# Performance work log

Hardware: AMD Instinct MI355X
Metric: run time of the kernel (lower is better)

Reference implementation:

```python
import jax, jax.numpy as jnp
import numpy as np
import math

N_HEAD = 16
HEAD_DIM = 64
LN_EPS = 1e-5
TEMP = 1.0

def _layernorm(x, scale, bias):
    # normalize over last dim (head_dim)
    mu = jnp.mean(x, axis=-1, keepdims=True)
    var = jnp.mean(jnp.square(x - mu), axis=-1, keepdims=True)
    return (x - mu) / jnp.sqrt(var + LN_EPS) * scale + bias

def setup_inputs() -> dict:
    key = jax.random.key(0)
    ks = jax.random.split(key, 3)
    B, S, C = 4, 2048, 1024
    x = jax.random.normal(ks[0], (B, S, C), dtype=jnp.float32)
    w_qkv = jax.random.normal(ks[1], (C, 3 * C), dtype=jnp.float32) * (C ** -0.5)
    w_proj = jax.random.normal(ks[2], (C, C), dtype=jnp.float32) * (C ** -0.5)
    return {
        "x": x,
        "w_qkv": w_qkv,
        "w_proj": w_proj,
        "q_scale": jnp.ones((HEAD_DIM,), jnp.float32),
        "q_bias": jnp.zeros((HEAD_DIM,), jnp.float32),
        "k_scale": jnp.ones((HEAD_DIM,), jnp.float32),
        "k_bias": jnp.zeros((HEAD_DIM,), jnp.float32),
    }

def reference(x, w_qkv, w_proj, q_scale, q_bias, k_scale, k_bias):
    B, S, C = x.shape
    H, D = N_HEAD, HEAD_DIM
    # qkv projection -> [B,S,3,H,D] -> [3,B,H,S,D]
    qkv = (x @ w_qkv).reshape(B, S, 3, H, D).transpose(2, 0, 3, 1, 4)
    q = _layernorm(qkv[0], q_scale, q_bias)
    k = _layernorm(qkv[1], k_scale, k_bias)
    v = qkv[2]
    # temperature-scaled logits, stable softmax
    inv = 1.0 / (math.sqrt(D) * max(TEMP, 1e-6))
    logits = jnp.einsum('bhqd,bhkd->bhqk', q, k) * inv
    att = jax.nn.softmax(logits, axis=-1)
    # entropy stats (track_stats=True path)
    s_raw = -jnp.sum(att * jnp.log(att + 1e-9), axis=-1)  # [B,H,S]
    batch_entropies = jnp.mean(s_raw / math.log(S), axis=(1, 2))  # [B]
    out = jnp.einsum('bhqk,bhkd->bhqd', att, v).transpose(0, 2, 1, 3).reshape(B, S, C)
    return out @ w_proj, batch_entropies
```

## Files before the change

kernel.cpp:

```cpp
#include <hip/hip_runtime.h>
#include <hip/hip_bf16.h>
#include <math.h>

#define CB 4
#define CS 2048
#define CC 1024
#define CH 16
#define CD 64
#define CBS (CB*CS)

typedef unsigned short u16;
typedef __bf16 bf16x8 __attribute__((ext_vector_type(8)));
typedef float f32x4 __attribute__((ext_vector_type(4)));
typedef float f32x16 __attribute__((ext_vector_type(16)));
typedef unsigned short u16x4 __attribute__((ext_vector_type(4)));
typedef unsigned short u16x8 __attribute__((ext_vector_type(8)));
typedef unsigned u32x2 __attribute__((ext_vector_type(2)));

__device__ __forceinline__ u16 f2bf(float f){
  union { float f; unsigned u; } v; v.f = f;
  unsigned r = v.u + 0x7FFFu + ((v.u >> 16) & 1u);
  return (u16)(r >> 16);
}
__device__ __forceinline__ unsigned pack2bf(float a, float b){
  __hip_bfloat162 h = __float22bfloat162_rn(make_float2(a, b));
  union { __hip_bfloat162 h; unsigned u; } c; c.h = h; return c.u;
}
__device__ __forceinline__ f32x4 mfma16(bf16x8 a, bf16x8 b, f32x4 c){
  return __builtin_amdgcn_mfma_f32_16x16x32_bf16(a, b, c, 0, 0, 0);
}
__device__ __forceinline__ f32x16 mfma32(bf16x8 a, bf16x8 b, f32x16 c){
  return __builtin_amdgcn_mfma_f32_32x32x16_bf16(a, b, c, 0, 0, 0);
}
__device__ __forceinline__ void gload16(const u16* g, u16* lds_base_uniform){
  __builtin_amdgcn_global_load_lds(
      (const __attribute__((address_space(1))) unsigned int*)g,
      (__attribute__((address_space(3))) unsigned int*)lds_base_uniform, 16, 0, 0);
}

__global__ __launch_bounds__(256) void convert_x_kernel(
    const float* __restrict__ x, u16* __restrict__ xb, float* __restrict__ zero4){
  if (blockIdx.x == 0 && threadIdx.x < 4) zero4[threadIdx.x] = 0.0f;
  size_t i = ((size_t)blockIdx.x*256 + threadIdx.x)*8;
  float4 a = *(const float4*)(x+i);
  float4 b = *(const float4*)(x+i+4);
  u16x8 o = { f2bf(a.x),f2bf(a.y),f2bf(a.z),f2bf(a.w),
              f2bf(b.x),f2bf(b.y),f2bf(b.z),f2bf(b.w) };
  *(u16x8*)(xb+i) = o;
}

template<int K, int N>
__global__ __launch_bounds__(256) void transpose_convert_kernel(
    const float* __restrict__ w, u16* __restrict__ wt){
  __shared__ u16 tile[64][65];
  const int nb = N/64;
  int tk0 = (blockIdx.x / nb) * 64;
  int tn0 = (blockIdx.x % nb) * 64;
  int t = threadIdx.x;
  for (int i = 0; i < 4; i++) {
    int r = i*16 + (t>>4);
    int c = (t&15)*4;
    float4 v = *(const float4*)(w + (size_t)(tk0+r)*N + tn0 + c);
    tile[c+0][r]=f2bf(v.x); tile[c+1][r]=f2bf(v.y);
    tile[c+2][r]=f2bf(v.z); tile[c+3][r]=f2bf(v.w);
  }
  __syncthreads();
  for (int i = 0; i < 4; i++) {
    int r = i*16 + (t>>4);
    int c = (t&15)*4;
    u16x4 o = { tile[r][c+0], tile[r][c+1], tile[r][c+2], tile[r][c+3] };
    *(u16x4*)(wt + (size_t)(tn0+r)*K + tk0 + c) = o;
  }
}

__global__ __launch_bounds__(256) void transpose_v_kernel(
    const u16* __restrict__ vb, u16* __restrict__ vtb){
  __shared__ u16 tile[64][72];
  int bh = blockIdx.x >> 5;
  int st = blockIdx.x & 31;
  int t = threadIdx.x;
  const u16* src = vb + (size_t)bh*CS*CD + (size_t)st*64*CD;
  int r = t>>2, c = (t&3)*16;
  *(u16x8*)&tile[r][c]   = *(const u16x8*)(src + (size_t)r*CD + c);
  *(u16x8*)&tile[r][c+8] = *(const u16x8*)(src + (size_t)r*CD + c + 8);
  __syncthreads();
  int d = t>>2, s = (t&3)*16;
  u16x8 o0, o1;
  for (int j=0;j<8;j++){ o0[j] = tile[s+j][d]; o1[j] = tile[s+8+j][d]; }
  u16* dst = vtb + (size_t)bh*CD*CS + (size_t)d*CS + st*64 + s;
  *(u16x8*)dst = o0;
  *(u16x8*)(dst+8) = o1;
}

__global__ __launch_bounds__(256, 2) void gemm_qkv_ln_kernel(
    const u16* __restrict__ xb, const u16* __restrict__ wqkvT,
    const float* __restrict__ qsc, const float* __restrict__ qbi,
    const float* __restrict__ ksc, const float* __restrict__ kbi,
    u16* __restrict__ qb, u16* __restrict__ kb, u16* __restrict__ vb){
  __shared__ u16 al[128*64];
  __shared__ u16 bl[128*64];
  int t = threadIdx.x;
  int wv = t >> 6, lane = t & 63, lo = lane & 15, q4 = lane >> 4;
  int m0 = blockIdx.x * 128;
  int n0 = blockIdx.y * 128;
  int srow = lane >> 3, scol = (lane & 7) * 8;
  const u16* ag = xb    + (size_t)(m0 + srow)*CC + scol;
  const u16* bg = wqkvT + (size_t)(n0 + srow)*CC + scol;

  f32x4 acc[2][8];
  for (int i=0;i<2;i++) for (int j=0;j<8;j++) acc[i][j] = (f32x4){0.f,0.f,0.f,0.f};

  for (int kk = 0; kk < 16; kk++){
    int k0 = kk * 64;
    for (int i = 0; i < 4; i++){
      int inst = i*4 + wv;
      gload16(ag + (size_t)inst*8*CC + k0, al + inst*512);
      gload16(bg + (size_t)inst*8*CC + k0, bl + inst*512);
    }
    __syncthreads();
    for (int ksI = 0; ksI < 2; ksI++){
      int koff = ksI*32 + q4*8;
      bf16x8 a0 = *(const bf16x8*)&al[(wv*32      + lo)*64 + koff];
      bf16x8 a1 = *(const bf16x8*)&al[(wv*32 + 16 + lo)*64 + koff];
      for (int nt=0; nt<8; nt++){
        bf16x8 b = *(const bf16x8*)&bl[(nt*16 + lo)*64 + koff];
        acc[0][nt] = mfma16(a0, b, acc[0][nt]);
        acc[1][nt] = mfma16(a1, b, acc[1][nt]);
      }
    }
    __syncthreads();
  }

  int three = n0 >> 10;
  int h0 = (n0 & 1023) >> 6;
  const float* scp = (three == 0) ? qsc : ksc;
  const float* bip = (three == 0) ? qbi : kbi;
  float outscale = (three == 0) ? 0.125f * 1.44269504088896f : 1.0f;
  u16* dst = (three == 0) ? qb : (three == 1 ? kb : vb);

  for (int rt = 0; rt < 2; rt++){
    int tg = m0 + wv*32 + rt*16 + q4*4;
    for (int hf = 0; hf < 2; hf++){
      int h = h0 + hf;
      for (int r = 0; r < 4; r++){
        int token = tg + r;
        int bb = token >> 11, ss = token & (CS-1);
        size_t base = (((size_t)(bb*CH + h))*CS + ss)*CD;
        if (three < 2){
          float s1 = 0.f, s2 = 0.f;
          for (int j=0;j<4;j++){ float v = acc[rt][hf*4+j][r]; s1 += v; s2 += v*v; }
          for (int off=8; off>=1; off>>=1){
            s1 += __shfl_xor(s1, off, 16);
            s2 += __shfl_xor(s2, off, 16);
          }
          float mean = s1 * (1.f/64.f);
          float var  = s2 * (1.f/64.f) - mean*mean;
          float rstd = rsqrtf(var + 1e-5f);
          for (int j=0;j<4;j++){
            int d = j*16 + lo;
            float v = (acc[rt][hf*4+j][r] - mean) * rstd * scp[d] + bip[d];
            dst[base + d] = f2bf(v * outscale);
          }
        } else {
          for (int j=0;j<4;j++){
            int d = j*16 + lo;
            dst[base + d] = f2bf(acc[rt][hf*4+j][r]);
          }
        }
      }
    }
  }
}

__global__ __launch_bounds__(256, 2) void attention_kernel(
    const u16* __restrict__ qb, const u16* __restrict__ kb,
    const u16* __restrict__ vtb, u16* __restrict__ attnb, float* __restrict__ ent){
  __shared__ __align__(16) u16 kl[3][32*64];
  __shared__ __align__(16) u16 vl[3][64*32];
  int t = threadIdx.x;
  int wv = t >> 6, lane = t & 63;
  int col = lane & 31, hi = lane >> 5;
  int n = blockIdx.x;
  int xc = n & 7, j = n >> 3;
  int bh = xc + 8*(j >> 4);
  int qt = j & 15;
  int bI = bh >> 4;
  int q0w = qt*128 + wv*32;
  const u16* qbp = qb  + (size_t)bh * CS * CD;
  const u16* kbp = kb  + (size_t)bh * CS * CD;
  const u16* vbp = vtb + (size_t)bh * CD * CS;

  int srow8  = lane >> 3, sl8 = lane & 7;
  int srow16 = lane >> 2, sl4 = lane & 3;

  bf16x8 qf[4];
  #pragma unroll
  for (int ks=0;ks<4;ks++)
    qf[ks] = *(const bf16x8*)(qbp + (size_t)(q0w + col)*CD + ks*16 + hi*8);

  f32x16 o[2];
  #pragma unroll
  for (int nt=0;nt<2;nt++)
    #pragma unroll
    for (int i=0;i<16;i++) o[nt][i] = 0.f;
  float zacc = 0.f, tacc = 0.f;

  auto stage = [&](int buf, int tile){
    int skn = tile*32;
    int krow  = wv*8 + srow8;
    int kslot = sl8 ^ srow8 ^ wv;
    gload16(kbp + (size_t)(skn + krow)*CD + kslot*8, &kl[buf][wv*512]);
    int vrow  = wv*16 + srow16;
    int vslot = sl4 ^ (srow16 & 3);
    gload16(vbp + (size_t)vrow*CS + skn + vslot*8, &vl[buf][wv*512]);
  };

  stage(0, 0);
  stage(1, 1);

  const int kkey = (col & 7) ^ (col >> 3);
  const int vkey = (col & 3);
  int cur = 0;

  for (int it = 0; it < 64; it++){
    if (it < 62){
      asm volatile("s_waitcnt vmcnt(2)" ::: "memory");
      __builtin_amdgcn_s_barrier();
      __builtin_amdgcn_sched_barrier(0);
      int nb = cur + 2; if (nb >= 3) nb -= 3;
      stage(nb, it + 2);
    } else if (it == 62){
      asm volatile("s_waitcnt vmcnt(2)" ::: "memory");
      __builtin_amdgcn_s_barrier();
      __builtin_amdgcn_sched_barrier(0);
    } else {
      asm volatile("s_waitcnt vmcnt(0)" ::: "memory");
      __builtin_amdgcn_s_barrier();
      __builtin_amdgcn_sched_barrier(0);
    }
    const u16* kc = &kl[cur][0];
    const u16* vc = &vl[cur][0];

    bf16x8 kfr[4], vfr[2][2];
    #pragma unroll
    for (int ks=0;ks<4;ks++)
      kfr[ks] = *(const bf16x8*)&kc[col*64 + (((2*ks+hi) ^ kkey)<<3)];
    #pragma unroll
    for (int nt=0;nt<2;nt++)
      #pragma unroll
      for (int ks=0;ks<2;ks++)
        vfr[nt][ks] = *(const bf16x8*)&vc[(nt*32+col)*32 + (((ks*2+hi) ^ vkey)<<3)];

    f32x16 sf;
    #pragma unroll
    for (int i=0;i<16;i++) sf[i] = 0.f;
    __builtin_amdgcn_s_setprio(1);
    #pragma unroll
    for (int ks=0;ks<4;ks++)
      sf = mfma32(kfr[ks], qf[ks], sf);
    __builtin_amdgcn_s_setprio(0);

    #pragma unroll
    for (int ksl=0; ksl<2; ksl++){
      float p[2][4];
      #pragma unroll
      for (int gg=0; gg<2; gg++){
        int g = 2*ksl + gg;
        float l0 = sf[g*4+0], l1 = sf[g*4+1],
              l2 = sf[g*4+2], l3 = sf[g*4+3];
        float p0 = __builtin_amdgcn_exp2f(l0);
        float p1 = __builtin_amdgcn_exp2f(l1);
        float p2 = __builtin_amdgcn_exp2f(l2);
        float p3 = __builtin_amdgcn_exp2f(l3);
        zacc += (p0+p1)+(p2+p3);
        tacc += (p0*l0+p1*l1)+(p2*l2+p3*l3);
        p[gg][0]=p0; p[gg][1]=p1; p[gg][2]=p2; p[gg][3]=p3;
      }
      unsigned x0 = pack2bf(p[0][0], p[0][1]);
      unsigned x1 = pack2bf(p[0][2], p[0][3]);
      unsigned y0 = pack2bf(p[1][0], p[1][1]);
      unsigned y1 = pack2bf(p[1][2], p[1][3]);
      u32x2 s0 = __builtin_amdgcn_permlane32_swap(x0, y0, false, false);
      u32x2 s1 = __builtin_amdgcn_permlane32_swap(x1, y1, false, false);
      union { unsigned u[4]; bf16x8 v; } ap;
      ap.u[0] = s0[0]; ap.u[1] = s1[0]; ap.u[2] = s0[1]; ap.u[3] = s1[1];
      __builtin_amdgcn_s_setprio(1);
      o[0] = mfma32(ap.v, vfr[0][ksl], o[0]);
      o[1] = mfma32(ap.v, vfr[1][ksl], o[1]);
      __builtin_amdgcn_s_setprio(0);
    }
    cur = (cur == 2) ? 0 : cur + 1;
  }

  float z2 = zacc + __shfl_xor(zacc, 32);
  float t2 = tacc + __shfl_xor(tacc, 32);
  float invz = 1.f / z2;

  float srowv = 0.69314718055995f * (__builtin_amdgcn_logf(z2) - t2 * invz);
  float ev = (hi == 0) ? srowv : 0.f;
  for (int off=1; off<=32; off<<=1) ev += __shfl_xor(ev, off);
  if (lane == 0){
    float entscale = 1.0f / ((float)CH * (float)CS * logf((float)CS));
    atomicAdd(&ent[bI], ev * entscale);
  }

  float izv[4][4];
  #pragma unroll
  for (int g=0; g<4; g++)
    #pragma unroll
    for (int r=0; r<4; r++)
      izv[g][r] = __shfl(invz, 8*g + 4*hi + r);

  u16* obase = attnb + ((size_t)bh*CS + q0w)*CD;
  #pragma unroll
  for (int nt=0;nt<2;nt++){
    #pragma unroll
    for (int g=0;g<4;g++){
      #pragma unroll
      for (int r=0;r<4;r++){
        int qrow = 8*g + 4*hi + r;
        obase[(size_t)qrow*CD + nt*32 + col] = f2bf(o[nt][g*4+r] * izv[g][r]);
      }
    }
  }
}

__global__ __launch_bounds__(256, 2) void gemm_out_kernel(
    const u16* __restrict__ attnH, const u16* __restrict__ wprojT,
    float* __restrict__ out){
  __shared__ u16 al[128*64];
  __shared__ u16 bl[128*64];
  int t = threadIdx.x;
  int wv = t >> 6, lane = t & 63, lo = lane & 15, q4 = lane >> 4;
  int m0 = blockIdx.x * 128;
  int n0 = blockIdx.y * 128;
  int b  = m0 >> 11, s0 = m0 & (CS-1);
  int srow = lane >> 3, scol = (lane & 7) * 8;
  const u16* bg = wprojT + (size_t)(n0 + srow)*CC + scol;

  f32x4 acc[2][8];
  for (int i=0;i<2;i++) for (int j=0;j<8;j++) acc[i][j] = (f32x4){0.f,0.f,0.f,0.f};

  for (int kk = 0; kk < 16; kk++){
    const u16* abase = attnH + ((size_t)(b*CH + kk)*CS + s0 + srow)*CD + scol;
    for (int i = 0; i < 4; i++){
      int inst = i*4 + wv;
      gload16(abase + (size_t)inst*8*CD, al + inst*512);
      gload16(bg + (size_t)inst*8*CC + kk*64, bl + inst*512);
    }
    __syncthreads();
    for (int ksI = 0; ksI < 2; ksI++){
      int koff = ksI*32 + q4*8;
      bf16x8 a0 = *(const bf16x8*)&al[(wv*32      + lo)*64 + koff];
      bf16x8 a1 = *(const bf16x8*)&al[(wv*32 + 16 + lo)*64 + koff];
      for (int nt=0; nt<8; nt++){
        bf16x8 b2 = *(const bf16x8*)&bl[(nt*16 + lo)*64 + koff];
        acc[0][nt] = mfma16(a0, b2, acc[0][nt]);
        acc[1][nt] = mfma16(a1, b2, acc[1][nt]);
      }
    }
    __syncthreads();
  }

  for (int rt=0;rt<2;rt++){
    for (int r=0;r<4;r++){
      int row = m0 + wv*32 + rt*16 + q4*4 + r;
      for (int nt=0;nt<8;nt++)
        out[(size_t)row*CC + n0 + nt*16 + lo] = acc[rt][nt][r];
    }
  }
}

extern "C" void kernel_launch(void* const* d_in, const int* in_sizes, int n_in,
                              void* d_out, int out_size, void* d_ws, size_t ws_size,
                              hipStream_t stream) {
  const float* x      = (const float*)d_in[0];
  const float* w_qkv  = (const float*)d_in[1];
  const float* w_proj = (const float*)d_in[2];
  const float* q_scale= (const float*)d_in[3];
  const float* q_bias = (const float*)d_in[4];
  const float* k_scale= (const float*)d_in[5];
  const float* k_bias = (const float*)d_in[6];
  float* out = (float*)d_out;
  float* ent = out + (size_t)CBS * CC;

  u16* xb     = (u16*)d_ws;
  u16* wqkvT  = xb     + (size_t)CBS*CC;
  u16* wprojT = wqkvT  + (size_t)3*CC*CC;
  u16* qb     = wprojT + (size_t)CC*CC;
  u16* kb     = qb + (size_t)CB*CH*CS*CD;
  u16* vb     = kb + (size_t)CB*CH*CS*CD;
  u16* vbT    = xb;
  u16* attn   = vb;

  convert_x_kernel<<<dim3(CBS*CC/(256*8)), 256, 0, stream>>>(x, xb, ent);
  transpose_convert_kernel<CC, 3*CC><<<dim3((CC/64)*(3*CC/64)), 256, 0, stream>>>(w_qkv, wqkvT);
  transpose_convert_kernel<CC, CC><<<dim3((CC/64)*(CC/64)), 256, 0, stream>>>(w_proj, wprojT);
  gemm_qkv_ln_kernel<<<dim3(CBS/128, 3*CC/128), 256, 0, stream>>>(
      xb, wqkvT, q_scale, q_bias, k_scale, k_bias, qb, kb, vb);
  transpose_v_kernel<<<dim3(CB*CH*(CS/64)), 256, 0, stream>>>(vb, vbT);
  attention_kernel<<<dim3(CB*CH*(CS/128)), 256, 0, stream>>>(qb, kb, vbT, attn, ent);
  gemm_out_kernel<<<dim3(CBS/128, CC/128), 256, 0, stream>>>(attn, wprojT, out);
}
```

Before: 344.9 us.

## Triple-buffer GEMM LDS tiles with async prefetch and XOR swizzle

Both projection GEMMs (the QKV+layernorm GEMM and the output projection) change from a single-buffered 64-wide K tile with two barriers per step to a three-stage ring of 32-wide K tiles. Global-to-LDS loads run two stages ahead and are waited on with explicit vmcnt counts, leaving one barrier per iteration. LDS tiles use an XOR swizzle to cut bank conflicts, and the MFMA section is run at raised wave priority. The aim is to hide global load latency behind MFMA work, at the cost of more iterations and more fragile hand-written wait counts.

```diff
diff --git a/kernel.cpp b/kernel.cpp
--- a/kernel.cpp
+++ b/kernel.cpp
@@ -97,38 +97,66 @@
     const float* __restrict__ qsc, const float* __restrict__ qbi,
     const float* __restrict__ ksc, const float* __restrict__ kbi,
     u16* __restrict__ qb, u16* __restrict__ kb, u16* __restrict__ vb){
-  __shared__ u16 al[128*64];
-  __shared__ u16 bl[128*64];
+  __shared__ __align__(16) u16 al[3][128*32];
+  __shared__ __align__(16) u16 bl[3][128*32];
   int t = threadIdx.x;
   int wv = t >> 6, lane = t & 63, lo = lane & 15, q4 = lane >> 4;
   int m0 = blockIdx.x * 128;
   int n0 = blockIdx.y * 128;
-  int srow = lane >> 3, scol = (lane & 7) * 8;
-  const u16* ag = xb    + (size_t)(m0 + srow)*CC + scol;
-  const u16* bg = wqkvT + (size_t)(n0 + srow)*CC + scol;
+  int lsA = (lane & 3) ^ ((lane >> 3) & 3);
+  const u16* ag0 = xb    + (size_t)(m0 + (lane>>2))*CC + lsA*8;
+  const u16* bg0 = wqkvT + (size_t)(n0 + (lane>>2))*CC + lsA*8;
 
   f32x4 acc[2][8];
-  for (int i=0;i<2;i++) for (int j=0;j<8;j++) acc[i][j] = (f32x4){0.f,0.f,0.f,0.f};
-
-  for (int kk = 0; kk < 16; kk++){
-    int k0 = kk * 64;
-    for (int i = 0; i < 4; i++){
-      int inst = i*4 + wv;
-      gload16(ag + (size_t)inst*8*CC + k0, al + inst*512);
-      gload16(bg + (size_t)inst*8*CC + k0, bl + inst*512);
-    }
-    __syncthreads();
-    for (int ksI = 0; ksI < 2; ksI++){
-      int koff = ksI*32 + q4*8;
-      bf16x8 a0 = *(const bf16x8*)&al[(wv*32      + lo)*64 + koff];
-      bf16x8 a1 = *(const bf16x8*)&al[(wv*32 + 16 + lo)*64 + koff];
-      for (int nt=0; nt<8; nt++){
-        bf16x8 b = *(const bf16x8*)&bl[(nt*16 + lo)*64 + koff];
-        acc[0][nt] = mfma16(a0, b, acc[0][nt]);
-        acc[1][nt] = mfma16(a1, b, acc[1][nt]);
-      }
-    }
-    __syncthreads();
+  #pragma unroll
+  for (int i=0;i<2;i++)
+    #pragma unroll
+    for (int j=0;j<8;j++) acc[i][j] = (f32x4){0.f,0.f,0.f,0.f};
+
+  auto stage = [&](int buf, int kk){
+    #pragma unroll
+    for (int cc=0; cc<2; cc++){
+      int c = wv*2 + cc;
+      gload16(ag0 + (size_t)c*16*CC + kk*32, &al[buf][c*512]);
+      gload16(bg0 + (size_t)c*16*CC + kk*32, &bl[buf][c*512]);
+    }
+  };
+
+  stage(0, 0);
+  stage(1, 1);
+  int cur = 0;
+  const int akey = (lo >> 1) & 3;
+
+  for (int kk = 0; kk < 32; kk++){
+    if (kk < 30){
+      asm volatile("s_waitcnt vmcnt(4)" ::: "memory");
+      __builtin_amdgcn_s_barrier();
+      __builtin_amdgcn_sched_barrier(0);
+      int nb = cur + 2; if (nb >= 3) nb -= 3;
+      stage(nb, kk + 2);
+    } else if (kk == 30){
+      asm volatile("s_waitcnt vmcnt(4)" ::: "memory");
+      __builtin_amdgcn_s_barrier();
+      __builtin_amdgcn_sched_barrier(0);
+    } else {
+      asm volatile("s_waitcnt vmcnt(0)" ::: "memory");
+      __builtin_amdgcn_s_barrier();
+      __builtin_amdgcn_sched_barrier(0);
+    }
+    const u16* ac = &al[cur][0];
+    const u16* bc = &bl[cur][0];
+    int soff = (q4 ^ akey) << 3;
+    bf16x8 a0 = *(const bf16x8*)&ac[(wv*32      + lo)*32 + soff];
+    bf16x8 a1 = *(const bf16x8*)&ac[(wv*32 + 16 + lo)*32 + soff];
+    __builtin_amdgcn_s_setprio(1);
+    #pragma unroll
+    for (int nt=0; nt<8; nt++){
+      bf16x8 b = *(const bf16x8*)&bc[(nt*16 + lo)*32 + soff];
+      acc[0][nt] = mfma16(a0, b, acc[0][nt]);
+      acc[1][nt] = mfma16(a1, b, acc[1][nt]);
+    }
+    __builtin_amdgcn_s_setprio(0);
+    cur = (cur == 2) ? 0 : cur + 1;
   }
 
   int three = n0 >> 10;
@@ -328,38 +356,68 @@
 __global__ __launch_bounds__(256, 2) void gemm_out_kernel(
     const u16* __restrict__ attnH, const u16* __restrict__ wprojT,
     float* __restrict__ out){
-  __shared__ u16 al[128*64];
-  __shared__ u16 bl[128*64];
+  __shared__ __align__(16) u16 al[3][128*32];
+  __shared__ __align__(16) u16 bl[3][128*32];
   int t = threadIdx.x;
   int wv = t >> 6, lane = t & 63, lo = lane & 15, q4 = lane >> 4;
   int m0 = blockIdx.x * 128;
   int n0 = blockIdx.y * 128;
   int b  = m0 >> 11, s0 = m0 & (CS-1);
-  int srow = lane >> 3, scol = (lane & 7) * 8;
-  const u16* bg = wprojT + (size_t)(n0 + srow)*CC + scol;
+  int lsA = (lane & 3) ^ ((lane >> 3) & 3);
+  const u16* bg0 = wprojT + (size_t)(n0 + (lane>>2))*CC + lsA*8;
 
   f32x4 acc[2][8];
-  for (int i=0;i<2;i++) for (int j=0;j<8;j++) acc[i][j] = (f32x4){0.f,0.f,0.f,0.f};
-
-  for (int kk = 0; kk < 16; kk++){
-    const u16* abase = attnH + ((size_t)(b*CH + kk)*CS + s0 + srow)*CD + scol;
-    for (int i = 0; i < 4; i++){
-      int inst = i*4 + wv;
-      gload16(abase + (size_t)inst*8*CD, al + inst*512);
-      gload16(bg + (size_t)inst*8*CC + kk*64, bl + inst*512);
-    }
-    __syncthreads();
-    for (int ksI = 0; ksI < 2; ksI++){
-      int koff = ksI*32 + q4*8;
-      bf16x8 a0 = *(const bf16x8*)&al[(wv*32      + lo)*64 + koff];
-      bf16x8 a1 = *(const bf16x8*)&al[(wv*32 + 16 + lo)*64 + koff];
-      for (int nt=0; nt<8; nt++){
-        bf16x8 b2 = *(const bf16x8*)&bl[(nt*16 + lo)*64 + koff];
-        acc[0][nt] = mfma16(a0, b2, acc[0][nt]);
-        acc[1][nt] = mfma16(a1, b2, acc[1][nt]);
-      }
-    }
-    __syncthreads();
+  #pragma unroll
+  for (int i=0;i<2;i++)
+    #pragma unroll
+    for (int j=0;j<8;j++) acc[i][j] = (f32x4){0.f,0.f,0.f,0.f};
+
+  auto stage = [&](int buf, int kk){
+    int h = kk >> 1, doff = (kk & 1) * 32;
+    #pragma unroll
+    for (int cc=0; cc<2; cc++){
+      int c = wv*2 + cc;
+      gload16(attnH + ((size_t)(b*CH + h)*CS + s0 + c*16 + (lane>>2))*CD + doff + lsA*8,
+              &al[buf][c*512]);
+      gload16(bg0 + (size_t)c*16*CC + kk*32, &bl[buf][c*512]);
+    }
+  };
+
+  stage(0, 0);
+  stage(1, 1);
+  int cur = 0;
+  const int akey = (lo >> 1) & 3;
+
+  for (int kk = 0; kk < 32; kk++){
+    if (kk < 30){
+      asm volatile("s_waitcnt vmcnt(4)" ::: "memory");
+      __builtin_amdgcn_s_barrier();
+      __builtin_amdgcn_sched_barrier(0);
+      int nb = cur + 2; if (nb >= 3) nb -= 3;
+      stage(nb, kk + 2);
+    } else if (kk == 30){
+      asm volatile("s_waitcnt vmcnt(4)" ::: "memory");
+      __builtin_amdgcn_s_barrier();
+      __builtin_amdgcn_sched_barrier(0);
+    } else {
+      asm volatile("s_waitcnt vmcnt(0)" ::: "memory");
+      __builtin_amdgcn_s_barrier();
+      __builtin_amdgcn_sched_barrier(0);
+    }
+    const u16* ac = &al[cur][0];
+    const u16* bc = &bl[cur][0];
+    int soff = (q4 ^ akey) << 3;
+    bf16x8 a0 = *(const bf16x8*)&ac[(wv*32      + lo)*32 + soff];
+    bf16x8 a1 = *(const bf16x8*)&ac[(wv*32 + 16 + lo)*32 + soff];
+    __builtin_amdgcn_s_setprio(1);
+    #pragma unroll
+    for (int nt=0; nt<8; nt++){
+      bf16x8 b2 = *(const bf16x8*)&bc[(nt*16 + lo)*32 + soff];
+      acc[0][nt] = mfma16(a0, b2, acc[0][nt]);
+      acc[1][nt] = mfma16(a1, b2, acc[1][nt]);
+    }
+    __builtin_amdgcn_s_setprio(0);
+    cur = (cur == 2) ? 0 : cur + 1;
   }
 
   for (int rt=0;rt<2;rt++){
```

New measurement: 335.3 us. 1.03x faster.
